# Performance work log

Hardware: AMD Instinct MI355X
Metric: run time of the kernel (lower is better)

## Reference

```python
import jax, jax.numpy as jnp
import numpy as np

MU = 255          # mu-law levels - 1
H = 64            # block_hidden_size
SKIP = 256        # skip_size
NL = 24           # num_layers
CYC = 6           # cycle_size -> dilation = 2**(i % CYC)
UPK = 4           # upsample conv kernel/stride
REP = 75          # upsample repeat
LF = 80           # local_features_size
B = 2
LLEN = 64                      # local (spectrogram) frames
SLEN = LLEN * UPK * REP        # 19200 signal samples


def setup_inputs() -> dict:
    key = jax.random.key(0)
    ks = jax.random.split(key, 16)
    s = 0.1
    rn = lambda k, shape: jax.random.normal(k, shape, jnp.float32) * s
    return {
        "local_features": jax.random.normal(ks[0], (B, LLEN, LF), jnp.float32),
        "gold_signal": jax.random.randint(ks[1], (B, SLEN), 0, MU + 1, jnp.int32),
        "embed_W": rn(ks[2], (H, MU + 1)),          # 1x1 conv (mu+1 -> H), as matrix
        "embed_b": rn(ks[3], (H,)),
        "up_W": rn(ks[4], (LF, LF, UPK)),           # ConvTranspose1d weight [in, out, k]
        "up_b": rn(ks[5], (LF,)),
        "cond_W": rn(ks[6], (NL * 2 * H, LF)),      # 1x1 conv LF -> NL*2H
        "cond_b": rn(ks[7], (NL * 2 * H,)),
        "dil_W": rn(ks[8], (NL, 2 * H, H, 2)),      # dilated causal conv, kernel 2
        "dil_b": rn(ks[9], (NL, 2 * H)),
        "skip_W": rn(ks[10], (NL, SKIP, H)),
        "skip_b": rn(ks[11], (NL, SKIP)),
        "res_W": rn(ks[12], (NL - 1, H, H)),        # no residual conv on last layer
        "res_b": rn(ks[13], (NL - 1, H)),
        "out_W1": rn(ks[14], (MU + 1, SKIP)),       # out conv 1 (no bias)
        "out_W2": rn(ks[15], (MU + 1, MU + 1)),     # out conv 2 (no bias)
    }


def reference(local_features, gold_signal, embed_W, embed_b, up_W, up_b,
              cond_W, cond_b, dil_W, dil_b, skip_W, skip_b, res_W, res_b,
              out_W1, out_W2):
    Bv = local_features.shape[0]
    # --- conditional features upsample ---
    x = jnp.transpose(local_features, (0, 2, 1))                     # [B, LF, Lloc]
    # ConvTranspose1d with kernel == stride == UPK: each frame emits UPK frames
    up = jnp.einsum('bct,cok->botk', x, up_W).reshape(Bv, LF, -1)    # [B, LF, Lloc*UPK]
    up = up + up_b[None, :, None]
    up = jnp.repeat(up, REP, axis=-1)                                # [B, LF, SLEN]
    cond = jnp.einsum('oc,bct->bot', cond_W, up) + cond_b[None, :, None]
    L = cond.shape[-1]
    cond = cond.reshape(Bv, NL, 2 * H, L)                            # per-layer 2H channels
    # --- embed mu-law one-hot signal (one-hot matmul == gather) ---
    sig = jnp.transpose(embed_W[:, gold_signal], (1, 0, 2)) + embed_b[None, :, None]  # [B, H, L]
    # --- residual blocks ---
    skip_sum = jnp.zeros((Bv, SKIP, L), cond.dtype)
    for i in range(NL):
        d = 2 ** (i % CYC)
        prev = jnp.pad(sig, ((0, 0), (0, 0), (d, 0)))[:, :, :L]      # causal shift by dilation
        a = (jnp.einsum('oc,bct->bot', dil_W[i, :, :, 0], prev)
             + jnp.einsum('oc,bct->bot', dil_W[i, :, :, 1], sig)
             + dil_b[i][None, :, None] + cond[:, i])
        z = jnp.tanh(a[:, :H]) * jax.nn.sigmoid(a[:, H:])            # gated activation
        skip_sum = skip_sum + jnp.einsum('oc,bct->bot', skip_W[i], z) + skip_b[i][None, :, None]
        if i < NL - 1:
            sig = sig + jnp.einsum('oc,bct->bot', res_W[i], z) + res_b[i][None, :, None]
    # --- output head: ReLU -> 1x1 -> ReLU -> 1x1 -> log_softmax over levels ---
    h = jax.nn.relu(skip_sum)
    h = jax.nn.relu(jnp.einsum('oc,bct->bot', out_W1, h))
    logits = jnp.einsum('oc,bct->bot', out_W2, h)
    return jax.nn.log_softmax(logits, axis=1)                        # [B, mu+1, SLEN]
```

## Files before the change

### kernel.cpp

```cpp
#include <hip/hip_runtime.h>
#include <math.h>

#define MU1   256
#define H     64
#define H2    128
#define SKIPC 256
#define NL    24
#define LF    80
#define UPK   4
#define REP   75
#define BB    2
#define LLEN  64
#define LL    19200

using bf16x8 = __attribute__((ext_vector_type(8))) short;
using bf16x4 = __attribute__((ext_vector_type(4))) short;
using f32x4  = __attribute__((ext_vector_type(4))) float;

__device__ __forceinline__ float b2f(short s) {
    union { unsigned u; float f; } v; v.u = ((unsigned)(unsigned short)s) << 16; return v.f;
}
__device__ __forceinline__ short f2b(float f) {
    union { float f; unsigned u; } v; v.f = f;
    unsigned r = (v.u + 0x7fff + ((v.u >> 16) & 1)) >> 16;
    return (short)r;
}

__global__ __launch_bounds__(256) void prep_kernel(
    const float* __restrict__ dil_W,  const float* __restrict__ skip_W,
    const float* __restrict__ res_W,  const float* __restrict__ embed_W,
    const float* __restrict__ embed_b,const float* __restrict__ cond_W,
    const float* __restrict__ out_W1, const float* __restrict__ out_W2,
    const float* __restrict__ skip_b,
    short* __restrict__ dil_Wb, short* __restrict__ skip_Wb,
    short* __restrict__ res_Wb, short* __restrict__ embed_allb,
    float* __restrict__ cond_Wt, short* __restrict__ W1b,
    short* __restrict__ W2b, float* __restrict__ sbsum)
{
    int idx = blockIdx.x * 256 + threadIdx.x;
    const int n1 = NL * 2 * H2 * H;
    const int n2 = NL * SKIPC * H;
    const int n3 = (NL - 1) * H * H;
    const int n4 = MU1 * H;
    const int n5 = LF * NL * H2;
    const int n6 = MU1 * SKIPC;
    const int n7 = MU1 * MU1;
    if (idx < n1) {
        int c = idx & 63; int o = (idx >> 6) & 127;
        int k = (idx >> 13) & 1; int i = idx >> 14;
        dil_Wb[idx] = f2b(dil_W[((i * H2 + o) * H + c) * 2 + k]);
        return;
    }
    idx -= n1;
    if (idx < n2) { skip_Wb[idx] = f2b(skip_W[idx]); return; }
    idx -= n2;
    if (idx < n3) { res_Wb[idx] = f2b(res_W[idx]); return; }
    idx -= n3;
    if (idx < n4) {
        int h = idx & 63; int g = idx >> 6;
        embed_allb[idx] = f2b(embed_W[h * MU1 + g] + embed_b[h]);
        return;
    }
    idx -= n4;
    if (idx < n5) {
        int o = idx % (NL * H2); int c = idx / (NL * H2);
        cond_Wt[idx] = cond_W[o * LF + c];
        return;
    }
    idx -= n5;
    if (idx < n6) { W1b[idx] = f2b(out_W1[idx]); return; }
    idx -= n6;
    if (idx < n7) { W2b[idx] = f2b(out_W2[idx]); return; }
    idx -= n7;
    if (idx < SKIPC) {
        float a = 0.f;
        for (int i = 0; i < NL; i++) a += skip_b[i * SKIPC + idx];
        sbsum[idx] = a;
        return;
    }
}

__global__ __launch_bounds__(256) void embed_kernel(
    const int* __restrict__ gold, const short* __restrict__ eW,
    short* __restrict__ sig)
{
    int idx = blockIdx.x * 256 + threadIdx.x;
    if (idx >= BB * LL * 8) return;
    int ch = idx & 7; int bt = idx >> 3;
    int g = gold[bt];
    *(bf16x8*)(sig + (size_t)bt * H + ch * 8) = *(const bf16x8*)(eW + g * H + ch * 8);
}

__global__ __launch_bounds__(256) void cond_kernel(
    const float* __restrict__ lf, const float* __restrict__ up_W,
    const float* __restrict__ up_b, const float* __restrict__ cond_Wt,
    const float* __restrict__ cond_b, const float* __restrict__ dil_b,
    float* __restrict__ condS)
{
    __shared__ float s_up[LF];
    int j = blockIdx.x;
    int ot = blockIdx.y;
    int b = blockIdx.z;
    int frame = j >> 2, k = j & 3;
    int tid = threadIdx.x;
    if (tid < LF) {
        float a = up_b[tid];
        const float* lfr = lf + (b * LLEN + frame) * LF;
        #pragma unroll 8
        for (int c = 0; c < LF; ++c) a += lfr[c] * up_W[(c * LF + tid) * UPK + k];
        s_up[tid] = a;
    }
    __syncthreads();
    int o = ot * 256 + tid;
    float a = cond_b[o] + dil_b[o];
    #pragma unroll 8
    for (int c = 0; c < LF; ++c) a += cond_Wt[c * 3072 + o] * s_up[c];
    condS[((size_t)(b * 256 + j)) * 3072 + o] = a;
}

template<int DA, int DB, bool LASTPAIR>
__global__ __launch_bounds__(256) void pair_mfma(
    const short* __restrict__ sig_in, short* __restrict__ sig_out,
    short* __restrict__ z_grp,
    const short* __restrict__ dil_Wb_all,
    const short* __restrict__ res_Wb_all,
    const float* __restrict__ res_b_all,
    const float* __restrict__ condS,
    int p)
{
    __shared__ __align__(16) short sa[144][72];
    __shared__ __align__(16) short sb[128][72];
    __shared__ __align__(16) short sz[128][72];
    __shared__ float scond[2][3][128];

    const int iA = 2 * p, iB = 2 * p + 1;
    const int ilA = iA & 7, ilB = iB & 7;
    const int b = blockIdx.y;
    const int t0 = blockIdx.x * 96;
    const int tid = threadIdx.x;
    const int w = tid >> 6;
    const int lane = tid & 63;
    const int lr = lane & 15, lg = lane >> 4;
    const int c0 = (t0 >= 32) ? (t0 - 32) / 75 : 0;

    {
        const short* basein = sig_in + (size_t)b * LL * H;
        #pragma unroll
        for (int it = 0; it < 5; ++it) {
            int task = tid + it * 256;
            if (task < 1152) {
                int r = task >> 3, ch = task & 7;
                int t = t0 - 48 + r;
                bf16x8 v = {};
                if (t >= 0) v = *(const bf16x8*)(basein + (size_t)t * H + ch * 8);
                *(bf16x8*)&sa[r][ch * 8] = v;
            }
        }
        #pragma unroll
        for (int it = 0; it < 3; ++it) {
            int task = tid + it * 256;
            int sel = task >= 384;
            int cj = (task - sel * 384) >> 7;
            int o = task & 127;
            int col = c0 + cj; col = col > 255 ? 255 : col;
            scond[sel][cj][o] = condS[((size_t)(b * 256 + col)) * 3072 + (iA + sel) * 128 + o];
        }
    }
    __syncthreads();

    {
        const short* dW = dil_Wb_all + (size_t)iA * 2 * H2 * H;
        f32x4 acc[2][8];
        #pragma unroll
        for (int m = 0; m < 2; ++m)
            #pragma unroll
            for (int n = 0; n < 8; ++n) acc[m][n] = (f32x4){0.f, 0.f, 0.f, 0.f};
        bf16x8 afA[2][4];
        #pragma unroll
        for (int m = 0; m < 2; ++m) {
            int rc = 16 + 16 * (2 * w + m) + lr;
            afA[m][0] = *(const bf16x8*)&sa[rc - DA][lg * 8];
            afA[m][1] = *(const bf16x8*)&sa[rc - DA][32 + lg * 8];
            afA[m][2] = *(const bf16x8*)&sa[rc][lg * 8];
            afA[m][3] = *(const bf16x8*)&sa[rc][32 + lg * 8];
        }
        #pragma unroll
        for (int n = 0; n < 8; ++n)
            #pragma unroll
            for (int kk = 0; kk < 4; ++kk) {
                bf16x8 bw = *(const bf16x8*)(dW + (((kk >> 1) * H2 + 16 * n + lr) * H) + (kk & 1) * 32 + lg * 8);
                acc[0][n] = __builtin_amdgcn_mfma_f32_16x16x32_bf16(afA[0][kk], bw, acc[0][n], 0, 0, 0);
                acc[1][n] = __builtin_amdgcn_mfma_f32_16x16x32_bf16(afA[1][kk], bw, acc[1][n], 0, 0, 0);
            }
        #pragma unroll
        for (int m = 0; m < 2; ++m)
            #pragma unroll
            for (int n = 0; n < 4; ++n)
                #pragma unroll
                for (int r = 0; r < 4; ++r) {
                    int relt = -32 + 16 * (2 * w + m) + 4 * lg + r;
                    int t = t0 + relt;
                    int o = 16 * n + lr;
                    short zb = 0;
                    if (t >= 0) {
                        int ci = t / 75 - c0;
                        float av = acc[m][n][r] + scond[0][ci][o];
                        float gv = acc[m][n + 4][r] + scond[0][ci][64 + o];
                        float th = 1.f - 2.f / (__expf(2.f * av) + 1.f);
                        float sg = 1.f / (1.f + __expf(-gv));
                        zb = f2b(th * sg);
                    }
                    sz[relt + 32][o] = zb;
                }
    }
    __syncthreads();

    #pragma unroll
    for (int it = 0; it < 3; ++it) {
        int task = tid + it * 256;
        int r = task >> 3, ch = task & 7;
        *(bf16x8*)(z_grp + ((size_t)(b * LL + t0 + r)) * 512 + ilA * 64 + ch * 8)
            = *(const bf16x8*)&sz[32 + r][ch * 8];
    }

    {
        const short* rW = res_Wb_all + (size_t)iA * H * H;
        const float* rb_ = res_b_all + (size_t)iA * H;
        f32x4 rac[2][4];
        #pragma unroll
        for (int m = 0; m < 2; ++m)
            #pragma unroll
            for (int n = 0; n < 4; ++n) rac[m][n] = (f32x4){0.f, 0.f, 0.f, 0.f};
        bf16x8 za[2][2];
        #pragma unroll
        for (int m = 0; m < 2; ++m) {
            int row = 16 * (2 * w + m) + lr;
            za[m][0] = *(const bf16x8*)&sz[row][lg * 8];
            za[m][1] = *(const bf16x8*)&sz[row][32 + lg * 8];
        }
        #pragma unroll
        for (int n = 0; n < 4; ++n)
            #pragma unroll
            for (int kk = 0; kk < 2; ++kk) {
                bf16x8 bw = *(const bf16x8*)(rW + (16 * n + lr) * H + kk * 32 + lg * 8);
                rac[0][n] = __builtin_amdgcn_mfma_f32_16x16x32_bf16(za[0][kk], bw, rac[0][n], 0, 0, 0);
                rac[1][n] = __builtin_amdgcn_mfma_f32_16x16x32_bf16(za[1][kk], bw, rac[1][n], 0, 0, 0);
            }
        #pragma unroll
        for (int n = 0; n < 4; ++n) {
            float rbv = rb_[16 * n + lr];
            #pragma unroll
            for (int m = 0; m < 2; ++m)
                #pragma unroll
                for (int r = 0; r < 4; ++r) {
                    int relt = -32 + 16 * (2 * w + m) + 4 * lg + r;
                    int t = t0 + relt;
                    int c = 16 * n + lr;
                    short vb = 0;
                    if (t >= 0) vb = f2b(b2f(sa[relt + 48][c]) + rac[m][n][r] + rbv);
                    sb[relt + 32][c] = vb;
                }
        }
    }
    __syncthreads();

    {
        const short* dW = dil_Wb_all + (size_t)iB * 2 * H2 * H;
        f32x4 accF[6], accG[6];
        #pragma unroll
        for (int m = 0; m < 6; ++m) { accF[m] = (f32x4){0.f,0.f,0.f,0.f}; accG[m] = (f32x4){0.f,0.f,0.f,0.f}; }
        bf16x8 bwF[4], bwG[4];
        #pragma unroll
        for (int kk = 0; kk < 4; ++kk) {
            int oF = 16 * w + lr;
            bwF[kk] = *(const bf16x8*)(dW + (((kk >> 1) * H2 + oF) * H) + (kk & 1) * 32 + lg * 8);
            bwG[kk] = *(const bf16x8*)(dW + (((kk >> 1) * H2 + 64 + oF) * H) + (kk & 1) * 32 + lg * 8);
        }
        #pragma unroll
        for (int m = 0; m < 6; ++m) {
            int rc = 32 + 16 * m + lr;
            bf16x8 af[4];
            af[0] = *(const bf16x8*)&sb[rc - DB][lg * 8];
            af[1] = *(const bf16x8*)&sb[rc - DB][32 + lg * 8];
            af[2] = *(const bf16x8*)&sb[rc][lg * 8];
            af[3] = *(const bf16x8*)&sb[rc][32 + lg * 8];
            #pragma unroll
            for (int kk = 0; kk < 4; ++kk)
                accF[m] = __builtin_amdgcn_mfma_f32_16x16x32_bf16(af[kk], bwF[kk], accF[m], 0, 0, 0);
            #pragma unroll
            for (int kk = 0; kk < 4; ++kk)
                accG[m] = __builtin_amdgcn_mfma_f32_16x16x32_bf16(af[kk], bwG[kk], accG[m], 0, 0, 0);
        }
        #pragma unroll
        for (int m = 0; m < 6; ++m)
            #pragma unroll
            for (int r = 0; r < 4; ++r) {
                int relt = 16 * m + 4 * lg + r;
                int t = t0 + relt;
                int o = 16 * w + lr;
                int ci = t / 75 - c0;
                float av = accF[m][r] + scond[1][ci][o];
                float gv = accG[m][r] + scond[1][ci][64 + o];
                float th = 1.f - 2.f / (__expf(2.f * av) + 1.f);
                float sg = 1.f / (1.f + __expf(-gv));
                sz[relt][o] = f2b(th * sg);
            }
    }
    __syncthreads();

    #pragma unroll
    for (int it = 0; it < 3; ++it) {
        int task = tid + it * 256;
        int r = task >> 3, ch = task & 7;
        *(bf16x8*)(z_grp + ((size_t)(b * LL + t0 + r)) * 512 + ilB * 64 + ch * 8)
            = *(const bf16x8*)&sz[r][ch * 8];
    }

    if (!LASTPAIR) {
        const short* rW = res_Wb_all + (size_t)iB * H * H;
        const float* rb_ = res_b_all + (size_t)iB * H;
        int c = 16 * w + lr;
        f32x4 rac[6];
        #pragma unroll
        for (int m = 0; m < 6; ++m) rac[m] = (f32x4){0.f, 0.f, 0.f, 0.f};
        bf16x8 bwR[2];
        bwR[0] = *(const bf16x8*)(rW + c * H + lg * 8);
        bwR[1] = *(const bf16x8*)(rW + c * H + 32 + lg * 8);
        #pragma unroll
        for (int m = 0; m < 6; ++m) {
            bf16x8 z0 = *(const bf16x8*)&sz[16 * m + lr][lg * 8];
            bf16x8 z1 = *(const bf16x8*)&sz[16 * m + lr][32 + lg * 8];
            rac[m] = __builtin_amdgcn_mfma_f32_16x16x32_bf16(z0, bwR[0], rac[m], 0, 0, 0);
            rac[m] = __builtin_amdgcn_mfma_f32_16x16x32_bf16(z1, bwR[1], rac[m], 0, 0, 0);
        }
        float rbv = rb_[c];
        #pragma unroll
        for (int m = 0; m < 6; ++m)
            #pragma unroll
            for (int r = 0; r < 4; ++r) {
                int relt = 16 * m + 4 * lg + r;
                sa[relt][c] = f2b(b2f(sb[relt + 32][c]) + rac[m][r] + rbv);
            }
        __syncthreads();
        #pragma unroll
        for (int it = 0; it < 3; ++it) {
            int task = tid + it * 256;
            int r = task >> 3, ch = task & 7;
            *(bf16x8*)(sig_out + ((size_t)(b * LL + t0 + r)) * H + ch * 8)
                = *(const bf16x8*)&sa[r][ch * 8];
        }
    }
}

template<bool G0>
__global__ __launch_bounds__(256) void skip_gemm(
    const short* __restrict__ z_grp, const short* __restrict__ sWb,
    float* __restrict__ skipS)
{
    __shared__ __align__(16) short s_a[64][136];
    const int b = blockIdx.y;
    const int t0 = blockIdx.x * 64;
    const int tid = threadIdx.x;
    const int w = tid >> 6;
    const int lane = tid & 63;
    const int lr = lane & 15, lg = lane >> 4;

    f32x4 acc[4][4];
    #pragma unroll
    for (int mt = 0; mt < 4; ++mt)
        #pragma unroll
        for (int nt = 0; nt < 4; ++nt) acc[mt][nt] = (f32x4){0.f, 0.f, 0.f, 0.f};

    for (int chunk = 0; chunk < 4; ++chunk) {
        __syncthreads();
        #pragma unroll
        for (int it = 0; it < 4; ++it) {
            int task = tid + it * 256;
            int r = task >> 4, ch = task & 15;
            *(bf16x8*)&s_a[r][ch * 8] =
                *(const bf16x8*)(z_grp + ((size_t)(b * LL + t0 + r)) * 512 + chunk * 128 + ch * 8);
        }
        __syncthreads();
        bf16x8 bw[4][4];
        #pragma unroll
        for (int nt = 0; nt < 4; ++nt)
            #pragma unroll
            for (int kk = 0; kk < 4; ++kk) {
                int layer = 2 * chunk + (kk >> 1);
                bw[nt][kk] = *(const bf16x8*)(sWb +
                    ((size_t)(layer * SKIPC + 64 * w + 16 * nt + lr)) * H + (kk & 1) * 32 + 8 * lg);
            }
        #pragma unroll
        for (int mt = 0; mt < 4; ++mt) {
            bf16x8 afr[4];
            #pragma unroll
            for (int kk = 0; kk < 4; ++kk)
                afr[kk] = *(const bf16x8*)&s_a[16 * mt + lr][32 * kk + 8 * lg];
            #pragma unroll
            for (int nt = 0; nt < 4; ++nt)
                #pragma unroll
                for (int kk = 0; kk < 4; ++kk)
                    acc[mt][nt] = __builtin_amdgcn_mfma_f32_16x16x32_bf16(afr[kk], bw[nt][kk], acc[mt][nt], 0, 0, 0);
        }
    }
    #pragma unroll
    for (int mt = 0; mt < 4; ++mt)
        #pragma unroll
        for (int nt = 0; nt < 4; ++nt) {
            int s = 64 * w + 16 * nt + lr;
            #pragma unroll
            for (int reg = 0; reg < 4; ++reg) {
                int t = t0 + 16 * mt + 4 * lg + reg;
                float* p = skipS + ((size_t)(b * LL + t)) * SKIPC + s;
                float v = acc[mt][nt][reg];
                if (!G0) v += *p;
                *p = v;
            }
        }
}

__global__ __launch_bounds__(256) void head_mfma(
    const float* __restrict__ skipS, const float* __restrict__ sbsum,
    const short* __restrict__ W1b, const short* __restrict__ W2b,
    float* __restrict__ out)
{
    __shared__ __align__(16) unsigned char smem[128 * 68 * 4];
    short (*s_x)[264] = (short(*)[264])smem;
    float (*s_o)[68]  = (float(*)[68])smem;
    __shared__ float s_red[4][64];
    __shared__ float s_sb[256];

    const int b = blockIdx.y;
    const int t0 = blockIdx.x * 64;
    const int tid = threadIdx.x;
    const int w = tid >> 6;
    const int lane = tid & 63;
    const int lr = lane & 15, lg = lane >> 4;

    s_sb[tid] = sbsum[tid];
    __syncthreads();

    #pragma unroll
    for (int it = 0; it < 16; ++it) {
        int task = tid + it * 256;
        int r = task >> 6, c4 = task & 63;
        f32x4 v = *(const f32x4*)(skipS + ((size_t)(b * LL + t0 + r)) * SKIPC + c4 * 4);
        bf16x4 o;
        #pragma unroll
        for (int j = 0; j < 4; ++j) o[j] = f2b(fmaxf(v[j] + s_sb[c4 * 4 + j], 0.f));
        *(bf16x4*)&s_x[r][c4 * 4] = o;
    }
    __syncthreads();

    f32x4 acc1[4][4];
    #pragma unroll
    for (int mt = 0; mt < 4; ++mt)
        #pragma unroll
        for (int nt = 0; nt < 4; ++nt) acc1[mt][nt] = (f32x4){0.f, 0.f, 0.f, 0.f};
    #pragma unroll
    for (int kk = 0; kk < 8; ++kk) {
        bf16x8 afr[4];
        #pragma unroll
        for (int mt = 0; mt < 4; ++mt)
            afr[mt] = *(const bf16x8*)&s_x[16 * mt + lr][32 * kk + 8 * lg];
        #pragma unroll
        for (int nt = 0; nt < 4; ++nt) {
            bf16x8 bw = *(const bf16x8*)(W1b + ((size_t)(64 * w + 16 * nt + lr)) * MU1 + 32 * kk + 8 * lg);
            #pragma unroll
            for (int mt = 0; mt < 4; ++mt)
                acc1[mt][nt] = __builtin_amdgcn_mfma_f32_16x16x32_bf16(afr[mt], bw, acc1[mt][nt], 0, 0, 0);
        }
    }
    __syncthreads();
    #pragma unroll
    for (int mt = 0; mt < 4; ++mt)
        #pragma unroll
        for (int nt = 0; nt < 4; ++nt)
            #pragma unroll
            for (int reg = 0; reg < 4; ++reg) {
                int tl = 16 * mt + 4 * lg + reg;
                int o = 64 * w + 16 * nt + lr;
                s_x[tl][o] = f2b(fmaxf(acc1[mt][nt][reg], 0.f));
            }
    __syncthreads();

    f32x4 acc2[4][4];
    #pragma unroll
    for (int mt = 0; mt < 4; ++mt)
        #pragma unroll
        for (int nt = 0; nt < 4; ++nt) acc2[mt][nt] = (f32x4){0.f, 0.f, 0.f, 0.f};
    #pragma unroll
    for (int kk = 0; kk < 8; ++kk) {
        bf16x8 afr[4];
        #pragma unroll
        for (int mt = 0; mt < 4; ++mt)
            afr[mt] = *(const bf16x8*)&s_x[16 * mt + lr][32 * kk + 8 * lg];
        #pragma unroll
        for (int nt = 0; nt < 4; ++nt) {
            bf16x8 bw = *(const bf16x8*)(W2b + ((size_t)(64 * w + 16 * nt + lr)) * MU1 + 32 * kk + 8 * lg);
            #pragma unroll
            for (int mt = 0; mt < 4; ++mt)
                acc2[mt][nt] = __builtin_amdgcn_mfma_f32_16x16x32_bf16(afr[mt], bw, acc2[mt][nt], 0, 0, 0);
        }
    }

    float mv[4][4];
    #pragma unroll
    for (int mt = 0; mt < 4; ++mt)
        #pragma unroll
        for (int reg = 0; reg < 4; ++reg) {
            float m = -3.4e38f;
            #pragma unroll
            for (int nt = 0; nt < 4; ++nt) m = fmaxf(m, acc2[mt][nt][reg]);
            #pragma unroll
            for (int off = 1; off <= 8; off <<= 1) m = fmaxf(m, __shfl_xor(m, off));
            int tl = 16 * mt + 4 * lg + reg;
            if (lr == 0) s_red[w][tl] = m;
        }
    __syncthreads();
    #pragma unroll
    for (int mt = 0; mt < 4; ++mt)
        #pragma unroll
        for (int reg = 0; reg < 4; ++reg) {
            int tl = 16 * mt + 4 * lg + reg;
            mv[mt][reg] = fmaxf(fmaxf(s_red[0][tl], s_red[1][tl]), fmaxf(s_red[2][tl], s_red[3][tl]));
        }
    __syncthreads();
    #pragma unroll
    for (int mt = 0; mt < 4; ++mt)
        #pragma unroll
        for (int reg = 0; reg < 4; ++reg) {
            float s = 0.f;
            #pragma unroll
            for (int nt = 0; nt < 4; ++nt) s += __expf(acc2[mt][nt][reg] - mv[mt][reg]);
            #pragma unroll
            for (int off = 1; off <= 8; off <<= 1) s += __shfl_xor(s, off);
            int tl = 16 * mt + 4 * lg + reg;
            if (lr == 0) s_red[w][tl] = s;
        }
    __syncthreads();
    #pragma unroll
    for (int mt = 0; mt < 4; ++mt)
        #pragma unroll
        for (int reg = 0; reg < 4; ++reg) {
            int tl = 16 * mt + 4 * lg + reg;
            float denom = s_red[0][tl] + s_red[1][tl] + s_red[2][tl] + s_red[3][tl];
            mv[mt][reg] = mv[mt][reg] + __logf(denom);
        }
    __syncthreads();

    #pragma unroll
    for (int pass = 0; pass < 2; ++pass) {
        if ((w >> 1) == pass) {
            #pragma unroll
            for (int mt = 0; mt < 4; ++mt)
                #pragma unroll
                for (int nt = 0; nt < 4; ++nt)
                    #pragma unroll
                    for (int reg = 0; reg < 4; ++reg) {
                        int ch = 64 * (w & 1) + 16 * nt + lr;
                        int tl = 16 * mt + 4 * lg + reg;
                        s_o[ch][tl] = acc2[mt][nt][reg] - mv[mt][reg];
                    }
        }
        __syncthreads();
        {
            int row = tid >> 1, half = tid & 1;
            float* op = out + ((size_t)(b * MU1 + pass * 128 + row)) * LL + t0 + half * 32;
            #pragma unroll
            for (int k = 0; k < 8; ++k)
                *(f32x4*)(op + 4 * k) = *(const f32x4*)&s_o[row][half * 32 + 4 * k];
        }
        __syncthreads();
    }
}

extern "C" void kernel_launch(void* const* d_in, const int* in_sizes, int n_in,
                              void* d_out, int out_size, void* d_ws, size_t ws_size,
                              hipStream_t stream)
{
    const float* lf      = (const float*)d_in[0];
    const int*   gold    = (const int*)  d_in[1];
    const float* embed_W = (const float*)d_in[2];
    const float* embed_b = (const float*)d_in[3];
    const float* up_W    = (const float*)d_in[4];
    const float* up_b    = (const float*)d_in[5];
    const float* cond_W  = (const float*)d_in[6];
    const float* cond_b  = (const float*)d_in[7];
    const float* dil_W   = (const float*)d_in[8];
    const float* dil_b   = (const float*)d_in[9];
    const float* skip_W  = (const float*)d_in[10];
    const float* skip_b  = (const float*)d_in[11];
    const float* res_W   = (const float*)d_in[12];
    const float* res_b   = (const float*)d_in[13];
    const float* W1      = (const float*)d_in[14];
    const float* W2      = (const float*)d_in[15];
    float* out = (float*)d_out;

    unsigned char* p = (unsigned char*)d_ws;
    short* sigA      = (short*)p; p += (size_t)BB * LL * H * 2;
    short* sigB      = (short*)p; p += (size_t)BB * LL * H * 2;
    short* z_grp     = (short*)p; p += (size_t)BB * LL * 512 * 2;
    float* skipS     = (float*)p; p += (size_t)BB * LL * SKIPC * 4;
    float* condS     = (float*)p; p += (size_t)BB * 256 * NL * H2 * 4;
    short* dil_Wb    = (short*)p; p += (size_t)NL * 2 * H2 * H * 2;
    short* skip_Wb   = (short*)p; p += (size_t)NL * SKIPC * H * 2;
    short* res_Wb    = (short*)p; p += (size_t)(NL - 1) * H * H * 2;
    short* embed_allb= (short*)p; p += (size_t)MU1 * H * 2;
    float* cond_Wt   = (float*)p; p += (size_t)LF * NL * H2 * 4;
    short* W1b       = (short*)p; p += (size_t)MU1 * SKIPC * 2;
    short* W2b       = (short*)p; p += (size_t)MU1 * MU1 * 2;
    float* sbsum     = (float*)p; p += (size_t)SKIPC * 4;

    const int prep_n = NL*2*H2*H + NL*SKIPC*H + (NL-1)*H*H + MU1*H + LF*NL*H2 + MU1*SKIPC + MU1*MU1 + SKIPC;
    prep_kernel<<<(prep_n + 255) / 256, 256, 0, stream>>>(
        dil_W, skip_W, res_W, embed_W, embed_b, cond_W, W1, W2, skip_b,
        dil_Wb, skip_Wb, res_Wb, embed_allb, cond_Wt, W1b, W2b, sbsum);

    embed_kernel<<<(BB * LL * 8 + 255) / 256, 256, 0, stream>>>(gold, embed_allb, sigA);

    cond_kernel<<<dim3(256, 12, BB), 256, 0, stream>>>(lf, up_W, up_b, cond_Wt, cond_b, dil_b, condS);

    short* si = sigA;
    short* so = sigB;
    dim3 pgrid(LL / 96, BB);
    dim3 sgrid(LL / 64, BB);
    for (int pp = 0; pp < 12; ++pp) {
        int r3 = pp % 3;
        if (r3 == 0)
            pair_mfma<1, 2, false><<<pgrid, 256, 0, stream>>>(si, so, z_grp, dil_Wb, res_Wb, res_b, condS, pp);
        else if (r3 == 1)
            pair_mfma<4, 8, false><<<pgrid, 256, 0, stream>>>(si, so, z_grp, dil_Wb, res_Wb, res_b, condS, pp);
        else if (pp == 11)
            pair_mfma<16, 32, true><<<pgrid, 256, 0, stream>>>(si, so, z_grp, dil_Wb, res_Wb, res_b, condS, pp);
        else
            pair_mfma<16, 32, false><<<pgrid, 256, 0, stream>>>(si, so, z_grp, dil_Wb, res_Wb, res_b, condS, pp);
        short* tmp = si; si = so; so = tmp;

        if ((pp & 3) == 3) {
            int g = pp >> 2;
            const short* sWb = skip_Wb + (size_t)g * 8 * SKIPC * H;
            if (g == 0)
                skip_gemm<true><<<sgrid, 256, 0, stream>>>(z_grp, sWb, skipS);
            else
                skip_gemm<false><<<sgrid, 256, 0, stream>>>(z_grp, sWb, skipS);
        }
    }

    head_mfma<<<sgrid, 256, 0, stream>>>(skipS, sbsum, W1b, W2b, out);
}
```

Baseline: 591.1 us.

## Widen pair kernel to 512 threads, batch skip GEMM over 12 layers, shrink head tile

Result: slower. 635.2 us (+7.5%).

```diff
diff --git a/kernel.cpp b/kernel.cpp
--- a/kernel.cpp
+++ b/kernel.cpp
@@ -119,14 +119,14 @@
 }
 
 template<int DA, int DB, bool LASTPAIR>
-__global__ __launch_bounds__(256) void pair_mfma(
+__global__ __launch_bounds__(512) void pair_mfma(
     const short* __restrict__ sig_in, short* __restrict__ sig_out,
-    short* __restrict__ z_grp,
+    short* __restrict__ z12,
     const short* __restrict__ dil_Wb_all,
     const short* __restrict__ res_Wb_all,
     const float* __restrict__ res_b_all,
     const float* __restrict__ condS,
-    int p)
+    int p, int slot)
 {
     __shared__ __align__(16) short sa[144][72];
     __shared__ __align__(16) short sb[128][72];
@@ -134,7 +134,6 @@
     __shared__ float scond[2][3][128];
 
     const int iA = 2 * p, iB = 2 * p + 1;
-    const int ilA = iA & 7, ilB = iB & 7;
     const int b = blockIdx.y;
     const int t0 = blockIdx.x * 96;
     const int tid = threadIdx.x;
@@ -146,8 +145,8 @@
     {
         const short* basein = sig_in + (size_t)b * LL * H;
         #pragma unroll
-        for (int it = 0; it < 5; ++it) {
-            int task = tid + it * 256;
+        for (int it = 0; it < 3; ++it) {
+            int task = tid + it * 512;
             if (task < 1152) {
                 int r = task >> 3, ch = task & 7;
                 int t = t0 - 48 + r;
@@ -157,128 +156,116 @@
             }
         }
         #pragma unroll
-        for (int it = 0; it < 3; ++it) {
-            int task = tid + it * 256;
-            int sel = task >= 384;
-            int cj = (task - sel * 384) >> 7;
-            int o = task & 127;
-            int col = c0 + cj; col = col > 255 ? 255 : col;
-            scond[sel][cj][o] = condS[((size_t)(b * 256 + col)) * 3072 + (iA + sel) * 128 + o];
+        for (int it = 0; it < 2; ++it) {
+            int task = tid + it * 512;
+            if (task < 768) {
+                int sel = task >= 384;
+                int cj = (task - sel * 384) >> 7;
+                int o = task & 127;
+                int col = c0 + cj; col = col > 255 ? 255 : col;
+                scond[sel][cj][o] = condS[((size_t)(b * 256 + col)) * 3072 + (iA + sel) * 128 + o];
+            }
         }
     }
     __syncthreads();
 
     {
         const short* dW = dil_Wb_all + (size_t)iA * 2 * H2 * H;
-        f32x4 acc[2][8];
-        #pragma unroll
-        for (int m = 0; m < 2; ++m)
-            #pragma unroll
-            for (int n = 0; n < 8; ++n) acc[m][n] = (f32x4){0.f, 0.f, 0.f, 0.f};
-        bf16x8 afA[2][4];
-        #pragma unroll
-        for (int m = 0; m < 2; ++m) {
-            int rc = 16 + 16 * (2 * w + m) + lr;
-            afA[m][0] = *(const bf16x8*)&sa[rc - DA][lg * 8];
-            afA[m][1] = *(const bf16x8*)&sa[rc - DA][32 + lg * 8];
-            afA[m][2] = *(const bf16x8*)&sa[rc][lg * 8];
-            afA[m][3] = *(const bf16x8*)&sa[rc][32 + lg * 8];
-        }
+        f32x4 acc[8];
+        #pragma unroll
+        for (int n = 0; n < 8; ++n) acc[n] = (f32x4){0.f, 0.f, 0.f, 0.f};
+        int rc = 16 + 16 * w + lr;
+        bf16x8 af[4];
+        af[0] = *(const bf16x8*)&sa[rc - DA][lg * 8];
+        af[1] = *(const bf16x8*)&sa[rc - DA][32 + lg * 8];
+        af[2] = *(const bf16x8*)&sa[rc][lg * 8];
+        af[3] = *(const bf16x8*)&sa[rc][32 + lg * 8];
         #pragma unroll
         for (int n = 0; n < 8; ++n)
             #pragma unroll
             for (int kk = 0; kk < 4; ++kk) {
                 bf16x8 bw = *(const bf16x8*)(dW + (((kk >> 1) * H2 + 16 * n + lr) * H) + (kk & 1) * 32 + lg * 8);
-                acc[0][n] = __builtin_amdgcn_mfma_f32_16x16x32_bf16(afA[0][kk], bw, acc[0][n], 0, 0, 0);
-                acc[1][n] = __builtin_amdgcn_mfma_f32_16x16x32_bf16(afA[1][kk], bw, acc[1][n], 0, 0, 0);
-            }
-        #pragma unroll
-        for (int m = 0; m < 2; ++m)
-            #pragma unroll
-            for (int n = 0; n < 4; ++n)
-                #pragma unroll
-                for (int r = 0; r < 4; ++r) {
-                    int relt = -32 + 16 * (2 * w + m) + 4 * lg + r;
-                    int t = t0 + relt;
-                    int o = 16 * n + lr;
-                    short zb = 0;
-                    if (t >= 0) {
-                        int ci = t / 75 - c0;
-                        float av = acc[m][n][r] + scond[0][ci][o];
-                        float gv = acc[m][n + 4][r] + scond[0][ci][64 + o];
-                        float th = 1.f - 2.f / (__expf(2.f * av) + 1.f);
-                        float sg = 1.f / (1.f + __expf(-gv));
-                        zb = f2b(th * sg);
-                    }
-                    sz[relt + 32][o] = zb;
+                acc[n] = __builtin_amdgcn_mfma_f32_16x16x32_bf16(af[kk], bw, acc[n], 0, 0, 0);
+            }
+        #pragma unroll
+        for (int n = 0; n < 4; ++n)
+            #pragma unroll
+            for (int r = 0; r < 4; ++r) {
+                int zrow = 16 * w + 4 * lg + r;
+                int t = t0 - 32 + zrow;
+                int o = 16 * n + lr;
+                short zb = 0;
+                if (t >= 0) {
+                    int ci = t / REP - c0;
+                    float av = acc[n][r] + scond[0][ci][o];
+                    float gv = acc[n + 4][r] + scond[0][ci][64 + o];
+                    float th = 1.f - 2.f / (__expf(2.f * av) + 1.f);
+                    float sg = 1.f / (1.f + __expf(-gv));
+                    zb = f2b(th * sg);
                 }
-    }
-    __syncthreads();
-
-    #pragma unroll
-    for (int it = 0; it < 3; ++it) {
-        int task = tid + it * 256;
-        int r = task >> 3, ch = task & 7;
-        *(bf16x8*)(z_grp + ((size_t)(b * LL + t0 + r)) * 512 + ilA * 64 + ch * 8)
-            = *(const bf16x8*)&sz[32 + r][ch * 8];
+                sz[zrow][o] = zb;
+            }
+    }
+    __syncthreads();
+
+    #pragma unroll
+    for (int it = 0; it < 2; ++it) {
+        int task = tid + it * 512;
+        if (task < 768) {
+            int r = task >> 3, ch = task & 7;
+            *(bf16x8*)(z12 + ((size_t)((slot * BB + b) * LL) + t0 + r) * 128 + ch * 8)
+                = *(const bf16x8*)&sz[32 + r][ch * 8];
+        }
     }
 
     {
         const short* rW = res_Wb_all + (size_t)iA * H * H;
         const float* rb_ = res_b_all + (size_t)iA * H;
-        f32x4 rac[2][4];
-        #pragma unroll
-        for (int m = 0; m < 2; ++m)
-            #pragma unroll
-            for (int n = 0; n < 4; ++n) rac[m][n] = (f32x4){0.f, 0.f, 0.f, 0.f};
-        bf16x8 za[2][2];
-        #pragma unroll
-        for (int m = 0; m < 2; ++m) {
-            int row = 16 * (2 * w + m) + lr;
-            za[m][0] = *(const bf16x8*)&sz[row][lg * 8];
-            za[m][1] = *(const bf16x8*)&sz[row][32 + lg * 8];
-        }
-        #pragma unroll
-        for (int n = 0; n < 4; ++n)
-            #pragma unroll
-            for (int kk = 0; kk < 2; ++kk) {
-                bf16x8 bw = *(const bf16x8*)(rW + (16 * n + lr) * H + kk * 32 + lg * 8);
-                rac[0][n] = __builtin_amdgcn_mfma_f32_16x16x32_bf16(za[0][kk], bw, rac[0][n], 0, 0, 0);
-                rac[1][n] = __builtin_amdgcn_mfma_f32_16x16x32_bf16(za[1][kk], bw, rac[1][n], 0, 0, 0);
-            }
+        f32x4 rac[4];
+        #pragma unroll
+        for (int n = 0; n < 4; ++n) rac[n] = (f32x4){0.f, 0.f, 0.f, 0.f};
+        int row = 16 * w + lr;
+        bf16x8 za0 = *(const bf16x8*)&sz[row][lg * 8];
+        bf16x8 za1 = *(const bf16x8*)&sz[row][32 + lg * 8];
+        #pragma unroll
+        for (int n = 0; n < 4; ++n) {
+            bf16x8 bw0 = *(const bf16x8*)(rW + (16 * n + lr) * H + lg * 8);
+            bf16x8 bw1 = *(const bf16x8*)(rW + (16 * n + lr) * H + 32 + lg * 8);
+            rac[n] = __builtin_amdgcn_mfma_f32_16x16x32_bf16(za0, bw0, rac[n], 0, 0, 0);
+            rac[n] = __builtin_amdgcn_mfma_f32_16x16x32_bf16(za1, bw1, rac[n], 0, 0, 0);
+        }
         #pragma unroll
         for (int n = 0; n < 4; ++n) {
             float rbv = rb_[16 * n + lr];
             #pragma unroll
-            for (int m = 0; m < 2; ++m)
-                #pragma unroll
-                for (int r = 0; r < 4; ++r) {
-                    int relt = -32 + 16 * (2 * w + m) + 4 * lg + r;
-                    int t = t0 + relt;
-                    int c = 16 * n + lr;
-                    short vb = 0;
-                    if (t >= 0) vb = f2b(b2f(sa[relt + 48][c]) + rac[m][n][r] + rbv);
-                    sb[relt + 32][c] = vb;
-                }
+            for (int r = 0; r < 4; ++r) {
+                int srow = 16 * w + 4 * lg + r;
+                int t = t0 - 32 + srow;
+                int c = 16 * n + lr;
+                short vb = 0;
+                if (t >= 0) vb = f2b(b2f(sa[srow + 16][c]) + rac[n][r] + rbv);
+                sb[srow][c] = vb;
+            }
         }
     }
     __syncthreads();
 
     {
         const short* dW = dil_Wb_all + (size_t)iB * 2 * H2 * H;
-        f32x4 accF[6], accG[6];
-        #pragma unroll
-        for (int m = 0; m < 6; ++m) { accF[m] = (f32x4){0.f,0.f,0.f,0.f}; accG[m] = (f32x4){0.f,0.f,0.f,0.f}; }
+        const int mh = w >> 2, nq = w & 3;
+        f32x4 accF[3], accG[3];
+        #pragma unroll
+        for (int m = 0; m < 3; ++m) { accF[m] = (f32x4){0.f,0.f,0.f,0.f}; accG[m] = (f32x4){0.f,0.f,0.f,0.f}; }
         bf16x8 bwF[4], bwG[4];
+        int oF = 16 * nq + lr;
         #pragma unroll
         for (int kk = 0; kk < 4; ++kk) {
-            int oF = 16 * w + lr;
             bwF[kk] = *(const bf16x8*)(dW + (((kk >> 1) * H2 + oF) * H) + (kk & 1) * 32 + lg * 8);
             bwG[kk] = *(const bf16x8*)(dW + (((kk >> 1) * H2 + 64 + oF) * H) + (kk & 1) * 32 + lg * 8);
         }
         #pragma unroll
-        for (int m = 0; m < 6; ++m) {
-            int rc = 32 + 16 * m + lr;
+        for (int m = 0; m < 3; ++m) {
+            int rc = 32 + 16 * (3 * mh + m) + lr;
             bf16x8 af[4];
             af[0] = *(const bf16x8*)&sb[rc - DB][lg * 8];
             af[1] = *(const bf16x8*)&sb[rc - DB][32 + lg * 8];
@@ -292,13 +279,13 @@
                 accG[m] = __builtin_amdgcn_mfma_f32_16x16x32_bf16(af[kk], bwG[kk], accG[m], 0, 0, 0);
         }
         #pragma unroll
-        for (int m = 0; m < 6; ++m)
+        for (int m = 0; m < 3; ++m)
             #pragma unroll
             for (int r = 0; r < 4; ++r) {
-                int relt = 16 * m + 4 * lg + r;
+                int relt = 16 * (3 * mh + m) + 4 * lg + r;
                 int t = t0 + relt;
-                int o = 16 * w + lr;
-                int ci = t / 75 - c0;
+                int o = 16 * nq + lr;
+                int ci = t / REP - c0;
                 float av = accF[m][r] + scond[1][ci][o];
                 float gv = accG[m][r] + scond[1][ci][64 + o];
                 float th = 1.f - 2.f / (__expf(2.f * av) + 1.f);
@@ -309,55 +296,60 @@
     __syncthreads();
 
     #pragma unroll
-    for (int it = 0; it < 3; ++it) {
-        int task = tid + it * 256;
-        int r = task >> 3, ch = task & 7;
-        *(bf16x8*)(z_grp + ((size_t)(b * LL + t0 + r)) * 512 + ilB * 64 + ch * 8)
-            = *(const bf16x8*)&sz[r][ch * 8];
+    for (int it = 0; it < 2; ++it) {
+        int task = tid + it * 512;
+        if (task < 768) {
+            int r = task >> 3, ch = task & 7;
+            *(bf16x8*)(z12 + ((size_t)((slot * BB + b) * LL) + t0 + r) * 128 + 64 + ch * 8)
+                = *(const bf16x8*)&sz[r][ch * 8];
+        }
     }
 
     if (!LASTPAIR) {
         const short* rW = res_Wb_all + (size_t)iB * H * H;
         const float* rb_ = res_b_all + (size_t)iB * H;
-        int c = 16 * w + lr;
-        f32x4 rac[6];
-        #pragma unroll
-        for (int m = 0; m < 6; ++m) rac[m] = (f32x4){0.f, 0.f, 0.f, 0.f};
-        bf16x8 bwR[2];
-        bwR[0] = *(const bf16x8*)(rW + c * H + lg * 8);
-        bwR[1] = *(const bf16x8*)(rW + c * H + 32 + lg * 8);
-        #pragma unroll
-        for (int m = 0; m < 6; ++m) {
-            bf16x8 z0 = *(const bf16x8*)&sz[16 * m + lr][lg * 8];
-            bf16x8 z1 = *(const bf16x8*)&sz[16 * m + lr][32 + lg * 8];
-            rac[m] = __builtin_amdgcn_mfma_f32_16x16x32_bf16(z0, bwR[0], rac[m], 0, 0, 0);
-            rac[m] = __builtin_amdgcn_mfma_f32_16x16x32_bf16(z1, bwR[1], rac[m], 0, 0, 0);
+        const int mh = w >> 2, nq = w & 3;
+        int c = 16 * nq + lr;
+        f32x4 rac[3];
+        #pragma unroll
+        for (int m = 0; m < 3; ++m) rac[m] = (f32x4){0.f, 0.f, 0.f, 0.f};
+        bf16x8 bwR0 = *(const bf16x8*)(rW + c * H + lg * 8);
+        bf16x8 bwR1 = *(const bf16x8*)(rW + c * H + 32 + lg * 8);
+        #pragma unroll
+        for (int m = 0; m < 3; ++m) {
+            int row = 16 * (3 * mh + m) + lr;
+            bf16x8 z0 = *(const bf16x8*)&sz[row][lg * 8];
+            bf16x8 z1 = *(const bf16x8*)&sz[row][32 + lg * 8];
+            rac[m] = __builtin_amdgcn_mfma_f32_16x16x32_bf16(z0, bwR0, rac[m], 0, 0, 0);
+            rac[m] = __builtin_amdgcn_mfma_f32_16x16x32_bf16(z1, bwR1, rac[m], 0, 0, 0);
         }
         float rbv = rb_[c];
         #pragma unroll
-        for (int m = 0; m < 6; ++m)
+        for (int m = 0; m < 3; ++m)
             #pragma unroll
             for (int r = 0; r < 4; ++r) {
-                int relt = 16 * m + 4 * lg + r;
+                int relt = 16 * (3 * mh + m) + 4 * lg + r;
                 sa[relt][c] = f2b(b2f(sb[relt + 32][c]) + rac[m][r] + rbv);
             }
         __syncthreads();
         #pragma unroll
-        for (int it = 0; it < 3; ++it) {
-            int task = tid + it * 256;
-            int r = task >> 3, ch = task & 7;
-            *(bf16x8*)(sig_out + ((size_t)(b * LL + t0 + r)) * H + ch * 8)
-                = *(const bf16x8*)&sa[r][ch * 8];
+        for (int it = 0; it < 2; ++it) {
+            int task = tid + it * 512;
+            if (task < 768) {
+                int r = task >> 3, ch = task & 7;
+                *(bf16x8*)(sig_out + ((size_t)(b * LL) + t0 + r) * H + ch * 8)
+                    = *(const bf16x8*)&sa[r][ch * 8];
+            }
         }
     }
 }
 
 template<bool G0>
-__global__ __launch_bounds__(256) void skip_gemm(
-    const short* __restrict__ z_grp, const short* __restrict__ sWb,
-    float* __restrict__ skipS)
+__global__ __launch_bounds__(256) void skip_slot(
+    const short* __restrict__ z12, const short* __restrict__ sWb,
+    float* __restrict__ skipS, int base)
 {
-    __shared__ __align__(16) short s_a[64][136];
+    __shared__ __align__(16) short s_a[2][64][136];
     const int b = blockIdx.y;
     const int t0 = blockIdx.x * 64;
     const int tid = threadIdx.x;
@@ -371,38 +363,45 @@
         #pragma unroll
         for (int nt = 0; nt < 4; ++nt) acc[mt][nt] = (f32x4){0.f, 0.f, 0.f, 0.f};
 
-    for (int chunk = 0; chunk < 4; ++chunk) {
+    #pragma unroll
+    for (int it = 0; it < 4; ++it) {
+        int task = tid + it * 256;
+        int r = task >> 4, ch = task & 15;
+        *(bf16x8*)&s_a[0][r][ch * 8] =
+            *(const bf16x8*)(z12 + ((size_t)(b * LL) + t0 + r) * 128 + ch * 8);
+    }
+    __syncthreads();
+
+    for (int ck = 0; ck < 6; ++ck) {
+        if (ck < 5) {
+            #pragma unroll
+            for (int it = 0; it < 4; ++it) {
+                int task = tid + it * 256;
+                int r = task >> 4, ch = task & 15;
+                *(bf16x8*)&s_a[(ck + 1) & 1][r][ch * 8] =
+                    *(const bf16x8*)(z12 + ((size_t)(((ck + 1) * BB + b) * LL) + t0 + r) * 128 + ch * 8);
+            }
+        }
+        const short (*buf)[136] = s_a[ck & 1];
+        #pragma unroll
+        for (int kk = 0; kk < 4; ++kk) {
+            bf16x8 afr[4];
+            #pragma unroll
+            for (int mt = 0; mt < 4; ++mt)
+                afr[mt] = *(const bf16x8*)&buf[16 * mt + lr][32 * kk + 8 * lg];
+            int layer = base + 2 * ck + (kk >> 1);
+            #pragma unroll
+            for (int nt = 0; nt < 4; ++nt) {
+                bf16x8 bw = *(const bf16x8*)(sWb +
+                    ((size_t)(layer * SKIPC + 64 * w + 16 * nt + lr)) * H + (kk & 1) * 32 + 8 * lg);
+                #pragma unroll
+                for (int mt = 0; mt < 4; ++mt)
+                    acc[mt][nt] = __builtin_amdgcn_mfma_f32_16x16x32_bf16(afr[mt], bw, acc[mt][nt], 0, 0, 0);
+            }
+        }
         __syncthreads();
-        #pragma unroll
-        for (int it = 0; it < 4; ++it) {
-            int task = tid + it * 256;
-            int r = task >> 4, ch = task & 15;
-            *(bf16x8*)&s_a[r][ch * 8] =
-                *(const bf16x8*)(z_grp + ((size_t)(b * LL + t0 + r)) * 512 + chunk * 128 + ch * 8);
-        }
-        __syncthreads();
-        bf16x8 bw[4][4];
-        #pragma unroll
-        for (int nt = 0; nt < 4; ++nt)
-            #pragma unroll
-            for (int kk = 0; kk < 4; ++kk) {
-                int layer = 2 * chunk + (kk >> 1);
-                bw[nt][kk] = *(const bf16x8*)(sWb +
-                    ((size_t)(layer * SKIPC + 64 * w + 16 * nt + lr)) * H + (kk & 1) * 32 + 8 * lg);
-            }
-        #pragma unroll
-        for (int mt = 0; mt < 4; ++mt) {
-            bf16x8 afr[4];
-            #pragma unroll
-            for (int kk = 0; kk < 4; ++kk)
-                afr[kk] = *(const bf16x8*)&s_a[16 * mt + lr][32 * kk + 8 * lg];
-            #pragma unroll
-            for (int nt = 0; nt < 4; ++nt)
-                #pragma unroll
-                for (int kk = 0; kk < 4; ++kk)
-                    acc[mt][nt] = __builtin_amdgcn_mfma_f32_16x16x32_bf16(afr[kk], bw[nt][kk], acc[mt][nt], 0, 0, 0);
-        }
-    }
+    }
+
     #pragma unroll
     for (int mt = 0; mt < 4; ++mt)
         #pragma unroll
@@ -424,14 +423,14 @@
     const short* __restrict__ W1b, const short* __restrict__ W2b,
     float* __restrict__ out)
 {
-    __shared__ __align__(16) unsigned char smem[128 * 68 * 4];
+    __shared__ __align__(16) unsigned char smem[18432];
     short (*s_x)[264] = (short(*)[264])smem;
-    float (*s_o)[68]  = (float(*)[68])smem;
-    __shared__ float s_red[4][64];
+    float (*s_o)[36]  = (float(*)[36])smem;
+    __shared__ float s_red[4][32];
     __shared__ float s_sb[256];
 
     const int b = blockIdx.y;
-    const int t0 = blockIdx.x * 64;
+    const int t0 = blockIdx.x * 32;
     const int tid = threadIdx.x;
     const int w = tid >> 6;
     const int lane = tid & 63;
@@ -441,7 +440,7 @@
     __syncthreads();
 
     #pragma unroll
-    for (int it = 0; it < 16; ++it) {
+    for (int it = 0; it < 8; ++it) {
         int task = tid + it * 256;
         int r = task >> 6, c4 = task & 63;
         f32x4 v = *(const f32x4*)(skipS + ((size_t)(b * LL + t0 + r)) * SKIPC + c4 * 4);
@@ -452,28 +451,28 @@
     }
     __syncthreads();
 
-    f32x4 acc1[4][4];
-    #pragma unroll
-    for (int mt = 0; mt < 4; ++mt)
+    f32x4 acc1[2][4];
+    #pragma unroll
+    for (int mt = 0; mt < 2; ++mt)
         #pragma unroll
         for (int nt = 0; nt < 4; ++nt) acc1[mt][nt] = (f32x4){0.f, 0.f, 0.f, 0.f};
     #pragma unroll
     for (int kk = 0; kk < 8; ++kk) {
-        bf16x8 afr[4];
-        #pragma unroll
-        for (int mt = 0; mt < 4; ++mt)
+        bf16x8 afr[2];
+        #pragma unroll
+        for (int mt = 0; mt < 2; ++mt)
             afr[mt] = *(const bf16x8*)&s_x[16 * mt + lr][32 * kk + 8 * lg];
         #pragma unroll
         for (int nt = 0; nt < 4; ++nt) {
             bf16x8 bw = *(const bf16x8*)(W1b + ((size_t)(64 * w + 16 * nt + lr)) * MU1 + 32 * kk + 8 * lg);
             #pragma unroll
-            for (int mt = 0; mt < 4; ++mt)
+            for (int mt = 0; mt < 2; ++mt)
                 acc1[mt][nt] = __builtin_amdgcn_mfma_f32_16x16x32_bf16(afr[mt], bw, acc1[mt][nt], 0, 0, 0);
         }
     }
     __syncthreads();
     #pragma unroll
-    for (int mt = 0; mt < 4; ++mt)
+    for (int mt = 0; mt < 2; ++mt)
         #pragma unroll
         for (int nt = 0; nt < 4; ++nt)
             #pragma unroll
@@ -484,29 +483,29 @@
             }
     __syncthreads();
 
-    f32x4 acc2[4][4];
-    #pragma unroll
-    for (int mt = 0; mt < 4; ++mt)
+    f32x4 acc2[2][4];
+    #pragma unroll
+    for (int mt = 0; mt < 2; ++mt)
         #pragma unroll
         for (int nt = 0; nt < 4; ++nt) acc2[mt][nt] = (f32x4){0.f, 0.f, 0.f, 0.f};
     #pragma unroll
     for (int kk = 0; kk < 8; ++kk) {
-        bf16x8 afr[4];
-        #pragma unroll
-        for (int mt = 0; mt < 4; ++mt)
+        bf16x8 afr[2];
+        #pragma unroll
+        for (int mt = 0; mt < 2; ++mt)
             afr[mt] = *(const bf16x8*)&s_x[16 * mt + lr][32 * kk + 8 * lg];
         #pragma unroll
         for (int nt = 0; nt < 4; ++nt) {
             bf16x8 bw = *(const bf16x8*)(W2b + ((size_t)(64 * w + 16 * nt + lr)) * MU1 + 32 * kk + 8 * lg);
             #pragma unroll
-            for (int mt = 0; mt < 4; ++mt)
+            for (int mt = 0; mt < 2; ++mt)
                 acc2[mt][nt] = __builtin_amdgcn_mfma_f32_16x16x32_bf16(afr[mt], bw, acc2[mt][nt], 0, 0, 0);
         }
     }
 
-    float mv[4][4];
-    #pragma unroll
-    for (int mt = 0; mt < 4; ++mt)
+    float mv[2][4];
+    #pragma unroll
+    for (int mt = 0; mt < 2; ++mt)
         #pragma unroll
         for (int reg = 0; reg < 4; ++reg) {
             float m = -3.4e38f;
@@ -519,7 +518,7 @@
         }
     __syncthreads();
     #pragma unroll
-    for (int mt = 0; mt < 4; ++mt)
+    for (int mt = 0; mt < 2; ++mt)
         #pragma unroll
         for (int reg = 0; reg < 4; ++reg) {
             int tl = 16 * mt + 4 * lg + reg;
@@ -527,7 +526,7 @@
         }
     __syncthreads();
     #pragma unroll
-    for (int mt = 0; mt < 4; ++mt)
+    for (int mt = 0; mt < 2; ++mt)
         #pragma unroll
         for (int reg = 0; reg < 4; ++reg) {
             float s = 0.f;
@@ -540,7 +539,7 @@
         }
     __syncthreads();
     #pragma unroll
-    for (int mt = 0; mt < 4; ++mt)
+    for (int mt = 0; mt < 2; ++mt)
         #pragma unroll
         for (int reg = 0; reg < 4; ++reg) {
             int tl = 16 * mt + 4 * lg + reg;
@@ -553,7 +552,7 @@
     for (int pass = 0; pass < 2; ++pass) {
         if ((w >> 1) == pass) {
             #pragma unroll
-            for (int mt = 0; mt < 4; ++mt)
+            for (int mt = 0; mt < 2; ++mt)
                 #pragma unroll
                 for (int nt = 0; nt < 4; ++nt)
                     #pragma unroll
@@ -566,10 +565,10 @@
         __syncthreads();
         {
             int row = tid >> 1, half = tid & 1;
-            float* op = out + ((size_t)(b * MU1 + pass * 128 + row)) * LL + t0 + half * 32;
-            #pragma unroll
-            for (int k = 0; k < 8; ++k)
-                *(f32x4*)(op + 4 * k) = *(const f32x4*)&s_o[row][half * 32 + 4 * k];
+            float* op = out + ((size_t)(b * MU1 + pass * 128 + row)) * LL + t0 + half * 16;
+            #pragma unroll
+            for (int k = 0; k < 4; ++k)
+                *(f32x4*)(op + 4 * k) = *(const f32x4*)&s_o[row][half * 16 + 4 * k];
         }
         __syncthreads();
     }
@@ -600,7 +599,7 @@
     unsigned char* p = (unsigned char*)d_ws;
     short* sigA      = (short*)p; p += (size_t)BB * LL * H * 2;
     short* sigB      = (short*)p; p += (size_t)BB * LL * H * 2;
-    short* z_grp     = (short*)p; p += (size_t)BB * LL * 512 * 2;
+    short* z12       = (short*)p; p += (size_t)6 * BB * LL * 128 * 2;
     float* skipS     = (float*)p; p += (size_t)BB * LL * SKIPC * 4;
     float* condS     = (float*)p; p += (size_t)BB * 256 * NL * H2 * 4;
     short* dil_Wb    = (short*)p; p += (size_t)NL * 2 * H2 * H * 2;
@@ -626,26 +625,23 @@
     dim3 pgrid(LL / 96, BB);
     dim3 sgrid(LL / 64, BB);
     for (int pp = 0; pp < 12; ++pp) {
+        int slot = pp % 6;
         int r3 = pp % 3;
         if (r3 == 0)
-            pair_mfma<1, 2, false><<<pgrid, 256, 0, stream>>>(si, so, z_grp, dil_Wb, res_Wb, res_b, condS, pp);
+            pair_mfma<1, 2, false><<<pgrid, 512, 0, stream>>>(si, so, z12, dil_Wb, res_Wb, res_b, condS, pp, slot);
         else if (r3 == 1)
-            pair_mfma<4, 8, false><<<pgrid, 256, 0, stream>>>(si, so, z_grp, dil_Wb, res_Wb, res_b, condS, pp);
+            pair_mfma<4, 8, false><<<pgrid, 512, 0, stream>>>(si, so, z12, dil_Wb, res_Wb, res_b, condS, pp, slot);
         else if (pp == 11)
-            pair_mfma<16, 32, true><<<pgrid, 256, 0, stream>>>(si, so, z_grp, dil_Wb, res_Wb, res_b, condS, pp);
+            pair_mfma<16, 32, true><<<pgrid, 512, 0, stream>>>(si, so, z12, dil_Wb, res_Wb, res_b, condS, pp, slot);
         else
-            pair_mfma<16, 32, false><<<pgrid, 256, 0, stream>>>(si, so, z_grp, dil_Wb, res_Wb, res_b, condS, pp);
+            pair_mfma<16, 32, false><<<pgrid, 512, 0, stream>>>(si, so, z12, dil_Wb, res_Wb, res_b, condS, pp, slot);
         short* tmp = si; si = so; so = tmp;
 
-        if ((pp & 3) == 3) {
-            int g = pp >> 2;
-            const short* sWb = skip_Wb + (size_t)g * 8 * SKIPC * H;
-            if (g == 0)
-                skip_gemm<true><<<sgrid, 256, 0, stream>>>(z_grp, sWb, skipS);
-            else
-                skip_gemm<false><<<sgrid, 256, 0, stream>>>(z_grp, sWb, skipS);
-        }
-    }
-
-    head_mfma<<<sgrid, 256, 0, stream>>>(skipS, sbsum, W1b, W2b, out);
-}
+        if (pp == 5)
+            skip_slot<true><<<sgrid, 256, 0, stream>>>(z12, skip_Wb, skipS, 0);
+    }
+
+    skip_slot<false><<<sgrid, 256, 0, stream>>>(z12, skip_Wb, skipS, 12);
+
+    head_mfma<<<dim3(LL / 32, BB), 256, 0, stream>>>(skipS, sbsum, W1b, W2b, out);
+}
```
